# Kernel optimization log

Hardware: AMD Instinct MI355X
Metric: run time of the kernel (lower is better)

Reference implementation:

```python
import jax, jax.numpy as jnp
import numpy as np

D_MODEL = 1024
N_HEADS = 16
HEAD_DIM = D_MODEL // N_HEADS
B, T = 4, 2048


def setup_inputs() -> dict:
    key = jax.random.key(0)
    ks = jax.random.split(key, 9)
    s = 1.0 / np.sqrt(D_MODEL)
    x = jax.random.normal(ks[0], (B, T, D_MODEL), dtype=jnp.float32)
    # causal mask: 1 = attend, 0 = blocked (masked_fill(mask == 0, -inf))
    mask = jnp.tril(jnp.ones((T, T), dtype=jnp.int32))[None, None, :, :]
    Wq = jax.random.uniform(ks[1], (D_MODEL, D_MODEL), jnp.float32, -s, s)
    bq = jax.random.uniform(ks[2], (D_MODEL,), jnp.float32, -s, s)
    Wk = jax.random.uniform(ks[3], (D_MODEL, D_MODEL), jnp.float32, -s, s)
    bk = jax.random.uniform(ks[4], (D_MODEL,), jnp.float32, -s, s)
    Wv = jax.random.uniform(ks[5], (D_MODEL, D_MODEL), jnp.float32, -s, s)
    bv = jax.random.uniform(ks[6], (D_MODEL,), jnp.float32, -s, s)
    Wo = jax.random.uniform(ks[7], (D_MODEL, D_MODEL), jnp.float32, -s, s)
    bo = jax.random.uniform(ks[8], (D_MODEL,), jnp.float32, -s, s)
    return {"x": x, "mask": mask, "Wq": Wq, "bq": bq, "Wk": Wk, "bk": bk,
            "Wv": Wv, "bv": bv, "Wo": Wo, "bo": bo}


def reference(x, mask, Wq, bq, Wk, bk, Wv, bv, Wo, bo):
    # nn.Linear: y = x @ W.T + b; here W stored as [in, out] so y = x @ W + b
    Bsz, Tlen, C = x.shape
    scale = jnp.sqrt(jnp.float32(HEAD_DIM))

    def split_heads(t):  # [B,T,C] -> [B,H,T,hd]
        return t.reshape(Bsz, Tlen, N_HEADS, HEAD_DIM).transpose(0, 2, 1, 3)

    Q = split_heads(x @ Wq + bq)
    K = split_heads(x @ Wk + bk)
    V = split_heads(x @ Wv + bv)

    scores = jnp.einsum("bhqd,bhkd->bhqk", Q, K) / scale
    scores = jnp.where(mask == 0, jnp.float32(-jnp.inf), scores)
    weights = jax.nn.softmax(scores, axis=-1)  # dropout is identity (eval/p=0)
    out = jnp.einsum("bhqk,bhkd->bhqd", weights, V)
    out = out.transpose(0, 2, 1, 3).reshape(Bsz, Tlen, C)
    return out @ Wo + bo
```

## Files before the change

### kernel.cpp

```cpp
#include <hip/hip_runtime.h>
#include <cstdint>
#include <cstddef>

#define B_SZ 4
#define T_SZ 2048
#define NH 16
#define HD 64
#define CD 1024
#define MROWS (B_SZ*T_SZ)
#define NEG_BIG (-1e30f)
#define Q_SCALE 0.180336880f

typedef __bf16 bf16x8 __attribute__((ext_vector_type(8)));
typedef __bf16 bf16x4 __attribute__((ext_vector_type(4)));
typedef short s16x4 __attribute__((ext_vector_type(4)));
typedef float f32x4 __attribute__((ext_vector_type(4)));

typedef __attribute__((address_space(3))) void* as3p;
typedef const __attribute__((address_space(1))) void* as1p;

__device__ __forceinline__ void glds16(const void* g, void* l) {
  __builtin_amdgcn_global_load_lds((as1p)g, (as3p)l, 16, 0, 0);
}

__global__ __launch_bounds__(256) void detect_dtype(const uint32_t* __restrict__ x,
                                                    int* __restrict__ flag) {
  __shared__ int cnt[256];
  const int t = threadIdx.x;
  int c = 0;
  for (int i = 0; i < 4; i++) {
    uint32_t w = x[t * 4 + i];
    uint32_t e = (w >> 7) & 0xFF;
    c += (e >= 100 && e <= 140) ? 1 : 0;
  }
  cnt[t] = c;
  __syncthreads();
  for (int s = 128; s > 0; s >>= 1) {
    if (t < s) cnt[t] += cnt[t + s];
    __syncthreads();
  }
  if (t == 0) flag[0] = (cnt[0] > 700) ? 1 : 0;
}

__device__ __forceinline__ bf16x8 cvt8(const void* src, int isbf, size_t i8) {
  bf16x8 o;
  if (isbf) {
    o = ((const bf16x8*)src)[i8];
  } else {
    const float4* s = (const float4*)((const float*)src + i8 * 8);
    float4 a = s[0], b = s[1];
    o[0] = (__bf16)a.x; o[1] = (__bf16)a.y; o[2] = (__bf16)a.z; o[3] = (__bf16)a.w;
    o[4] = (__bf16)b.x; o[5] = (__bf16)b.y; o[6] = (__bf16)b.z; o[7] = (__bf16)b.w;
  }
  return o;
}

__global__ __launch_bounds__(256) void conv_in(const void* __restrict__ src,
                                               const int* __restrict__ flag,
                                               __bf16* __restrict__ dst, int n8) {
  int i = blockIdx.x * 256 + threadIdx.x;
  if (i >= n8) return;
  ((bf16x8*)dst)[i] = cvt8(src, flag[0], i);
}

struct Ptr4 { const void* s[4]; __bf16* d[4]; };

__global__ __launch_bounds__(256) void conv_b4(Ptr4 p, const int* __restrict__ flag) {
  int i = threadIdx.x;
  if (i >= CD / 8) return;
  int which = blockIdx.x;
  ((bf16x8*)p.d[which])[i] = cvt8(p.s[which], flag[0], i);
}

__global__ __launch_bounds__(256) void transpose_conv4(Ptr4 p,
                                                       const int* __restrict__ flag) {
  __shared__ __align__(16) __bf16 tile[64 * 72];
  const void* W = p.s[blockIdx.z];
  __bf16* WT = p.d[blockIdx.z];
  const int t = threadIdx.x;
  const int r0 = blockIdx.y * 64, c0 = blockIdx.x * 64;
  const int rr = t >> 3, c8 = (t & 7) * 8;
  const int isbf = flag[0];
  for (int pp = 0; pp < 2; pp++) {
    int r = pp * 32 + rr;
    *(bf16x8*)(tile + r * 72 + c8) =
        cvt8(W, isbf, ((size_t)(r0 + r) * CD + c0 + c8) / 8);
  }
  __syncthreads();
  for (int pp = 0; pp < 2; pp++) {
    int cc = pp * 32 + rr;
    bf16x8 o;
    for (int j = 0; j < 8; j++) o[j] = tile[(c8 + j) * 72 + cc];
    *(bf16x8*)(WT + (size_t)(c0 + cc) * CD + r0 + c8) = o;
  }
}

__global__ __launch_bounds__(256) void gemm_qkv(
    const __bf16* __restrict__ A, const __bf16* __restrict__ BT,
    const __bf16* __restrict__ bias,
    __bf16* __restrict__ Qb, __bf16* __restrict__ Kb, __bf16* __restrict__ Vt) {
  __shared__ __align__(16) __bf16 As[128 * 64];
  __shared__ __align__(16) __bf16 Bs[128 * 64];
  const int tid = threadIdx.x;
  const int w = tid >> 6, lane = tid & 63;
  const int l15 = lane & 15, quad = lane >> 4;
  const int wm = w & 1, wn = w >> 1;
  const int bm = blockIdx.y, bn = blockIdx.x;

  f32x4 acc[4][4];
  for (int i = 0; i < 4; i++)
    for (int j = 0; j < 4; j++) acc[i][j] = (f32x4)0.f;

  const int srow = lane >> 3, scol = (lane & 7) * 8;
  const __bf16* Abase = A + (size_t)(bm * 128) * CD;
  const __bf16* Bbase = BT + (size_t)(bn * 128) * CD;

  for (int k0 = 0; k0 < CD; k0 += 64) {
    __syncthreads();
    for (int p = 0; p < 4; p++) {
      int seg = p * 4 + w;
      int row = seg * 8 + srow;
      glds16(Abase + (size_t)row * CD + k0 + scol, (char*)As + seg * 1024);
      glds16(Bbase + (size_t)row * CD + k0 + scol, (char*)Bs + seg * 1024);
    }
    __syncthreads();
    for (int kc = 0; kc < 2; kc++) {
      const int koff = kc * 32 + quad * 8;
      bf16x8 af[4], bfr[4];
      for (int mt = 0; mt < 4; mt++)
        af[mt] = *(const bf16x8*)(As + (wm * 64 + mt * 16 + l15) * 64 + koff);
      for (int nt = 0; nt < 4; nt++)
        bfr[nt] = *(const bf16x8*)(Bs + (wn * 64 + nt * 16 + l15) * 64 + koff);
      for (int mt = 0; mt < 4; mt++)
        for (int nt = 0; nt < 4; nt++)
          acc[mt][nt] = __builtin_amdgcn_mfma_f32_16x16x32_bf16(
              af[mt], bfr[nt], acc[mt][nt], 0, 0, 0);
    }
  }

  for (int nt = 0; nt < 4; nt++) {
    int col = bn * 128 + wn * 64 + nt * 16 + l15;
    int seg = col >> 10;
    int c = col & 1023, h = c >> 6, d = c & 63;
    float bv = (float)bias[col];
    for (int mt = 0; mt < 4; mt++) {
      int row0 = bm * 128 + wm * 64 + mt * 16 + quad * 4;
      int b = row0 >> 11, tok0 = row0 & 2047;
      if (seg == 2) {
        bf16x4 o;
        for (int r = 0; r < 4; r++) o[r] = (__bf16)(acc[mt][nt][r] + bv);
        *(bf16x4*)(Vt + ((size_t)((b << 4) + h) * HD + d) * T_SZ + tok0) = o;
      } else {
        __bf16* dst = (seg == 0) ? Qb : Kb;
        float sc = (seg == 0) ? Q_SCALE : 1.f;
        for (int r = 0; r < 4; r++) {
          float v = (acc[mt][nt][r] + bv) * sc;
          dst[((size_t)(b * NH + h) * T_SZ + tok0 + r) * HD + d] = (__bf16)v;
        }
      }
    }
  }
}

__global__ __launch_bounds__(256) void gemm_out(
    const __bf16* __restrict__ A, const __bf16* __restrict__ BT,
    const __bf16* __restrict__ bias, void* __restrict__ Out,
    const int* __restrict__ flag) {
  __shared__ __align__(16) __bf16 As[128 * 64];
  __shared__ __align__(16) __bf16 Bs[128 * 64];
  const int tid = threadIdx.x;
  const int w = tid >> 6, lane = tid & 63;
  const int l15 = lane & 15, quad = lane >> 4;
  const int wm = w & 1, wn = w >> 1;
  const int bm = blockIdx.y, bn = blockIdx.x;

  f32x4 acc[4][4];
  for (int i = 0; i < 4; i++)
    for (int j = 0; j < 4; j++) acc[i][j] = (f32x4)0.f;

  const int srow = lane >> 3, scol = (lane & 7) * 8;
  const __bf16* Abase = A + (size_t)(bm * 128) * CD;
  const __bf16* Bbase = BT + (size_t)(bn * 128) * CD;

  for (int k0 = 0; k0 < CD; k0 += 64) {
    __syncthreads();
    for (int p = 0; p < 4; p++) {
      int seg = p * 4 + w;
      int row = seg * 8 + srow;
      glds16(Abase + (size_t)row * CD + k0 + scol, (char*)As + seg * 1024);
      glds16(Bbase + (size_t)row * CD + k0 + scol, (char*)Bs + seg * 1024);
    }
    __syncthreads();
    for (int kc = 0; kc < 2; kc++) {
      const int koff = kc * 32 + quad * 8;
      bf16x8 af[4], bfr[4];
      for (int mt = 0; mt < 4; mt++)
        af[mt] = *(const bf16x8*)(As + (wm * 64 + mt * 16 + l15) * 64 + koff);
      for (int nt = 0; nt < 4; nt++)
        bfr[nt] = *(const bf16x8*)(Bs + (wn * 64 + nt * 16 + l15) * 64 + koff);
      for (int mt = 0; mt < 4; mt++)
        for (int nt = 0; nt < 4; nt++)
          acc[mt][nt] = __builtin_amdgcn_mfma_f32_16x16x32_bf16(
              af[mt], bfr[nt], acc[mt][nt], 0, 0, 0);
    }
  }

  const int isbf = flag[0];
  for (int nt = 0; nt < 4; nt++) {
    int col = bn * 128 + wn * 64 + nt * 16 + l15;
    float bv = (float)bias[col];
    for (int mt = 0; mt < 4; mt++) {
      int row0 = bm * 128 + wm * 64 + mt * 16 + quad * 4;
      if (isbf) {
        for (int r = 0; r < 4; r++)
          ((__bf16*)Out)[(size_t)(row0 + r) * CD + col] =
              (__bf16)(acc[mt][nt][r] + bv);
      } else {
        for (int r = 0; r < 4; r++)
          ((float*)Out)[(size_t)(row0 + r) * CD + col] = acc[mt][nt][r] + bv;
      }
    }
  }
}

__global__ __launch_bounds__(512, 4) void attn(
    const __bf16* __restrict__ Q, const __bf16* __restrict__ K,
    const __bf16* __restrict__ Vt, __bf16* __restrict__ Y) {
  __shared__ __align__(16) __bf16 Ks[2][64 * 72];
  __shared__ __align__(16) __bf16 Vs[2][64 * 76];

  const int tid = threadIdx.x, w = tid >> 6, lane = tid & 63;
  const int l15 = lane & 15, quad = lane >> 4;
  const int lid = blockIdx.x + 8 * blockIdx.y;
  const int bh = lid & 63;
  const int pairi = lid >> 6;

  const __bf16* Qbh = Q + (size_t)bh * T_SZ * HD;
  const __bf16* Kbh = K + (size_t)bh * T_SZ * HD;
  const __bf16* Vbh = Vt + (size_t)bh * HD * T_SZ;

  const int srow = tid >> 3;
  const int scol = (tid & 7) * 8;
  const int b = bh >> 4, h = bh & 15;

  for (int ph = 0; ph < 2; ph++) {
    const int tq = ph ? (15 - pairi) : pairi;
    const int q0 = tq * 128;
    const int niter = 2 * tq + 2;
    const int qw = q0 + w * 16;

    __syncthreads();
    *(bf16x8*)(Ks[0] + srow * 72 + scol) =
        *(const bf16x8*)(Kbh + (size_t)srow * HD + scol);
    {
      bf16x8 v0 = *(const bf16x8*)(Vbh + (size_t)srow * T_SZ + scol);
      *(bf16x4*)(Vs[0] + srow * 76 + scol)     = ((bf16x4*)&v0)[0];
      *(bf16x4*)(Vs[0] + srow * 76 + scol + 4) = ((bf16x4*)&v0)[1];
    }

    bf16x8 aq[2];
    for (int kc = 0; kc < 2; kc++)
      aq[kc] = *(const bf16x8*)(
          Qbh + (size_t)(qw + l15) * HD + kc * 32 + quad * 8);

    f32x4 acco[4];
    for (int dt = 0; dt < 4; dt++) acco[dt] = (f32x4)0.f;
    float m_ = NEG_BIG, l_ = 0.f;

    for (int it = 0; it < niter; it++) {
      const int cur = it & 1;
      const int kv0 = it * 64;
      __syncthreads();

      bf16x8 kn, vn;
      const bool havenext = (it + 1 < niter);
      if (havenext) {
        int kv1 = kv0 + 64;
        kn = *(const bf16x8*)(Kbh + (size_t)(kv1 + srow) * HD + scol);
        vn = *(const bf16x8*)(Vbh + (size_t)srow * T_SZ + kv1 + scol);
      }

      if (kv0 <= qw + 15) {
        const __bf16* Ksc = Ks[cur];
        const __bf16* Vsc = Vs[cur];

        f32x4 accs[4];
        for (int nt = 0; nt < 4; nt++) accs[nt] = (f32x4)0.f;
        for (int kc = 0; kc < 2; kc++)
          for (int nt = 0; nt < 4; nt++) {
            bf16x8 ak = *(const bf16x8*)(Ksc + (nt * 16 + l15) * 72 + kc * 32 + quad * 8);
            accs[nt] = __builtin_amdgcn_mfma_f32_16x16x32_bf16(
                ak, aq[kc], accs[nt], 0, 0, 0);
          }

        if (kv0 + 63 > qw) {
          int qg = qw + l15;
          for (int nt = 0; nt < 4; nt++) {
            int kg0 = kv0 + nt * 16 + quad * 4;
            for (int r = 0; r < 4; r++)
              if (kg0 + r > qg) accs[nt][r] = NEG_BIG;
          }
        }

        float a0 = fmaxf(fmaxf(accs[0][0], accs[0][1]),
                         fmaxf(accs[0][2], accs[0][3]));
        float a1 = fmaxf(fmaxf(accs[1][0], accs[1][1]),
                         fmaxf(accs[1][2], accs[1][3]));
        float a2 = fmaxf(fmaxf(accs[2][0], accs[2][1]),
                         fmaxf(accs[2][2], accs[2][3]));
        float a3 = fmaxf(fmaxf(accs[3][0], accs[3][1]),
                         fmaxf(accs[3][2], accs[3][3]));
        float mloc = fmaxf(fmaxf(a0, a1), fmaxf(a2, a3));
        mloc = fmaxf(mloc, __shfl_xor(mloc, 16));
        mloc = fmaxf(mloc, __shfl_xor(mloc, 32));

        if (!__all(mloc <= m_)) {
          float mnew = fmaxf(m_, mloc);
          float alpha = exp2f(m_ - mnew);
          m_ = mnew;
          l_ *= alpha;
          for (int dt = 0; dt < 4; dt++)
            for (int r = 0; r < 4; r++) acco[dt][r] *= alpha;
        }

        float rs = 0.f;
        bf16x4 pf[4];
        for (int nt = 0; nt < 4; nt++)
          for (int r = 0; r < 4; r++) {
            float p = exp2f(accs[nt][r] - m_);
            rs += p;
            pf[nt][r] = (__bf16)p;
          }
        rs += __shfl_xor(rs, 16);
        rs += __shfl_xor(rs, 32);
        l_ += rs;

        for (int nt = 0; nt < 4; nt++)
          for (int dt = 0; dt < 4; dt++) {
            bf16x4 av = *(const bf16x4*)(Vsc + (dt * 16 + l15) * 76 + nt * 16 + quad * 4);
            acco[dt] = __builtin_amdgcn_mfma_f32_16x16x16bf16_1k(
                *(const s16x4*)&av, *(const s16x4*)&pf[nt], acco[dt], 0, 0, 0);
          }
      }

      if (havenext) {
        int nb = cur ^ 1;
        *(bf16x8*)(Ks[nb] + srow * 72 + scol) = kn;
        *(bf16x4*)(Vs[nb] + srow * 76 + scol)     = ((bf16x4*)&vn)[0];
        *(bf16x4*)(Vs[nb] + srow * 76 + scol + 4) = ((bf16x4*)&vn)[1];
      }
    }

    {
      float rcp = 1.f / l_;
      int qg = qw + l15;
      size_t base = ((size_t)(b * T_SZ + qg)) * CD + h * HD + quad * 4;
      for (int dt = 0; dt < 4; dt++) {
        bf16x4 o;
        for (int r = 0; r < 4; r++) o[r] = (__bf16)(acco[dt][r] * rcp);
        *(bf16x4*)(Y + base + dt * 16) = o;
      }
    }
  }
}

extern "C" void kernel_launch(void* const* d_in, const int* in_sizes, int n_in,
                              void* d_out, int out_size, void* d_ws, size_t ws_size,
                              hipStream_t stream) {
  (void)in_sizes; (void)n_in; (void)out_size; (void)ws_size;
  const void* x  = d_in[0];
  const void* Wq = d_in[2];
  const void* bq = d_in[3];
  const void* Wk = d_in[4];
  const void* bk = d_in[5];
  const void* Wv = d_in[6];
  const void* bv = d_in[7];
  const void* Wo = d_in[8];
  const void* bo = d_in[9];

  char* ws = (char*)d_ws;
  const size_t MB = 1024 * 1024;
  __bf16* WqkvT = (__bf16*)(ws + 0 * MB);
  __bf16* WoT   = (__bf16*)(ws + 6 * MB);
  __bf16* bqkvc = (__bf16*)(ws + 8 * MB);
  __bf16* boc   = (__bf16*)(ws + 8 * MB + 8192);
  int*    flag  = (int*)   (ws + 8 * MB + 65536);
  __bf16* xc    = (__bf16*)(ws + 9 * MB);
  __bf16* Qb    = (__bf16*)(ws + 25 * MB);
  __bf16* Kb    = (__bf16*)(ws + 41 * MB);
  __bf16* Vt_g  = (__bf16*)(ws + 57 * MB);
  __bf16* Yb    = xc;

  dim3 tb(256);
  detect_dtype<<<1, tb, 0, stream>>>((const uint32_t*)x, flag);

  conv_in<<<4096, tb, 0, stream>>>(x, flag, xc, MROWS * CD / 8);
  Ptr4 pb = {{bq, bk, bv, bo}, {bqkvc, bqkvc + CD, bqkvc + 2 * CD, boc}};
  conv_b4<<<4, tb, 0, stream>>>(pb, flag);
  Ptr4 pw = {{Wq, Wk, Wv, Wo},
             {WqkvT, WqkvT + (size_t)CD * CD, WqkvT + 2 * (size_t)CD * CD, WoT}};
  transpose_conv4<<<dim3(16, 16, 4), tb, 0, stream>>>(pw, flag);

  gemm_qkv<<<dim3(24, MROWS / 128), tb, 0, stream>>>(xc, WqkvT, bqkvc, Qb, Kb, Vt_g);

  attn<<<dim3(8, B_SZ * NH), dim3(512), 0, stream>>>(Qb, Kb, Vt_g, Yb);

  gemm_out<<<dim3(CD / 128, MROWS / 128), tb, 0, stream>>>(Yb, WoT, boc, d_out, flag);
}
```

Measured before the change: 314.5 us.

## Compute softmax row sums via MFMA, swizzle K LDS layout, use fast exp2

The softmax denominator is now accumulated by an extra MFMA against a vector of ones, which replaces the per-lane sum and the cross-lane shuffle reductions. The K tile in LDS drops its padding in favour of an XOR swizzle to avoid bank conflicts. exp2f calls become the hardware exp2 builtin, and the max reduction is rebalanced into a flatter tree. This trades VALU and shuffle work for one extra MFMA per sub-tile, and the row sum is now taken from bf16-rounded probabilities, which may change accuracy slightly.

```diff
diff --git a/kernel.cpp b/kernel.cpp
--- a/kernel.cpp
+++ b/kernel.cpp
@@ -226,7 +226,7 @@
 __global__ __launch_bounds__(512, 4) void attn(
     const __bf16* __restrict__ Q, const __bf16* __restrict__ K,
     const __bf16* __restrict__ Vt, __bf16* __restrict__ Y) {
-  __shared__ __align__(16) __bf16 Ks[2][64 * 72];
+  __shared__ __align__(16) __bf16 Ks[2][64 * 64];
   __shared__ __align__(16) __bf16 Vs[2][64 * 76];
 
   const int tid = threadIdx.x, w = tid >> 6, lane = tid & 63;
@@ -241,7 +241,11 @@
 
   const int srow = tid >> 3;
   const int scol = (tid & 7) * 8;
+  const int kwcol = scol ^ ((srow & 7) * 8);
   const int b = bh >> 4, h = bh & 15;
+
+  bf16x4 ones;
+  for (int r = 0; r < 4; r++) ones[r] = (__bf16)1.0f;
 
   for (int ph = 0; ph < 2; ph++) {
     const int tq = ph ? (15 - pairi) : pairi;
@@ -250,7 +254,7 @@
     const int qw = q0 + w * 16;
 
     __syncthreads();
-    *(bf16x8*)(Ks[0] + srow * 72 + scol) =
+    *(bf16x8*)(Ks[0] + srow * 64 + kwcol) =
         *(const bf16x8*)(Kbh + (size_t)srow * HD + scol);
     {
       bf16x8 v0 = *(const bf16x8*)(Vbh + (size_t)srow * T_SZ + scol);
@@ -265,7 +269,8 @@
 
     f32x4 acco[4];
     for (int dt = 0; dt < 4; dt++) acco[dt] = (f32x4)0.f;
-    float m_ = NEG_BIG, l_ = 0.f;
+    f32x4 accl = (f32x4)0.f;
+    float m_ = NEG_BIG;
 
     for (int it = 0; it < niter; it++) {
       const int cur = it & 1;
@@ -286,9 +291,11 @@
 
         f32x4 accs[4];
         for (int nt = 0; nt < 4; nt++) accs[nt] = (f32x4)0.f;
+        const int swz = (l15 & 7) * 8;
         for (int kc = 0; kc < 2; kc++)
           for (int nt = 0; nt < 4; nt++) {
-            bf16x8 ak = *(const bf16x8*)(Ksc + (nt * 16 + l15) * 72 + kc * 32 + quad * 8);
+            bf16x8 ak = *(const bf16x8*)(
+                Ksc + (nt * 16 + l15) * 64 + ((kc * 32 + quad * 8) ^ swz));
             accs[nt] = __builtin_amdgcn_mfma_f32_16x16x32_bf16(
                 ak, aq[kc], accs[nt], 0, 0, 0);
           }
@@ -302,57 +309,52 @@
           }
         }
 
-        float a0 = fmaxf(fmaxf(accs[0][0], accs[0][1]),
-                         fmaxf(accs[0][2], accs[0][3]));
-        float a1 = fmaxf(fmaxf(accs[1][0], accs[1][1]),
-                         fmaxf(accs[1][2], accs[1][3]));
-        float a2 = fmaxf(fmaxf(accs[2][0], accs[2][1]),
-                         fmaxf(accs[2][2], accs[2][3]));
-        float a3 = fmaxf(fmaxf(accs[3][0], accs[3][1]),
-                         fmaxf(accs[3][2], accs[3][3]));
-        float mloc = fmaxf(fmaxf(a0, a1), fmaxf(a2, a3));
+        float t0 = fmaxf(fmaxf(accs[0][0], accs[0][1]), accs[0][2]);
+        float t1 = fmaxf(fmaxf(accs[0][3], accs[1][0]), accs[1][1]);
+        float t2 = fmaxf(fmaxf(accs[1][2], accs[1][3]), accs[2][0]);
+        float t3 = fmaxf(fmaxf(accs[2][1], accs[2][2]), accs[2][3]);
+        float t4 = fmaxf(fmaxf(accs[3][0], accs[3][1]), accs[3][2]);
+        float t5 = fmaxf(fmaxf(t0, t1), t2);
+        float t6 = fmaxf(fmaxf(t3, t4), accs[3][3]);
+        float mloc = fmaxf(t5, t6);
         mloc = fmaxf(mloc, __shfl_xor(mloc, 16));
         mloc = fmaxf(mloc, __shfl_xor(mloc, 32));
 
         if (!__all(mloc <= m_)) {
           float mnew = fmaxf(m_, mloc);
-          float alpha = exp2f(m_ - mnew);
+          float alpha = __builtin_amdgcn_exp2f(m_ - mnew);
           m_ = mnew;
-          l_ *= alpha;
+          accl[0] *= alpha;
           for (int dt = 0; dt < 4; dt++)
             for (int r = 0; r < 4; r++) acco[dt][r] *= alpha;
         }
 
-        float rs = 0.f;
         bf16x4 pf[4];
         for (int nt = 0; nt < 4; nt++)
-          for (int r = 0; r < 4; r++) {
-            float p = exp2f(accs[nt][r] - m_);
-            rs += p;
-            pf[nt][r] = (__bf16)p;
-          }
-        rs += __shfl_xor(rs, 16);
-        rs += __shfl_xor(rs, 32);
-        l_ += rs;
-
-        for (int nt = 0; nt < 4; nt++)
+          for (int r = 0; r < 4; r++)
+            pf[nt][r] = (__bf16)__builtin_amdgcn_exp2f(accs[nt][r] - m_);
+
+        for (int nt = 0; nt < 4; nt++) {
+          accl = __builtin_amdgcn_mfma_f32_16x16x16bf16_1k(
+              *(const s16x4*)&ones, *(const s16x4*)&pf[nt], accl, 0, 0, 0);
           for (int dt = 0; dt < 4; dt++) {
             bf16x4 av = *(const bf16x4*)(Vsc + (dt * 16 + l15) * 76 + nt * 16 + quad * 4);
             acco[dt] = __builtin_amdgcn_mfma_f32_16x16x16bf16_1k(
                 *(const s16x4*)&av, *(const s16x4*)&pf[nt], acco[dt], 0, 0, 0);
           }
+        }
       }
 
       if (havenext) {
         int nb = cur ^ 1;
-        *(bf16x8*)(Ks[nb] + srow * 72 + scol) = kn;
+        *(bf16x8*)(Ks[nb] + srow * 64 + kwcol) = kn;
         *(bf16x4*)(Vs[nb] + srow * 76 + scol)     = ((bf16x4*)&vn)[0];
         *(bf16x4*)(Vs[nb] + srow * 76 + scol + 4) = ((bf16x4*)&vn)[1];
       }
     }
 
     {
-      float rcp = 1.f / l_;
+      float rcp = 1.f / accl[0];
       int qg = qw + l15;
       size_t base = ((size_t)(b * T_SZ + qg)) * CD + h * HD + quad * 4;
       for (int dt = 0; dt < 4; dt++) {
```

After: 297.3 us. 1.06x faster.
